# Kernel tuning notes

Hardware: AMD Instinct MI355X
Metric: run time of the kernel (lower is better)

Reference implementation:

```python
import jax, jax.numpy as jnp
import numpy as np

B, S, IN_SIZE = 16, 2000, 128
D, H, FF, OUT = 256, 2, 256, 64


def setup_inputs() -> dict:
    key = jax.random.key(0)
    ks = jax.random.split(key, 8)
    u = lambda k, shape: jax.random.uniform(k, shape, minval=-0.1, maxval=0.1, dtype=jnp.float32)
    g = lambda k, shape, fan: jax.random.normal(k, shape, dtype=jnp.float32) * (1.0 / np.sqrt(fan))
    return {
        "src": jax.random.normal(ks[0], (B, S, IN_SIZE), dtype=jnp.float32),
        "enc_w": u(ks[1], (D, IN_SIZE)), "enc_b": jnp.zeros((D,), jnp.float32),
        "in_proj_w": g(ks[2], (3 * D, D), D), "in_proj_b": jnp.zeros((3 * D,), jnp.float32),
        "out_proj_w": g(ks[3], (D, D), D), "out_proj_b": jnp.zeros((D,), jnp.float32),
        "ln1_g": jnp.ones((D,), jnp.float32), "ln1_b": jnp.zeros((D,), jnp.float32),
        "ff1_w": g(ks[4], (FF, D), D), "ff1_b": jnp.zeros((FF,), jnp.float32),
        "ff2_w": g(ks[5], (D, FF), FF), "ff2_b": jnp.zeros((D,), jnp.float32),
        "ln2_g": jnp.ones((D,), jnp.float32), "ln2_b": jnp.zeros((D,), jnp.float32),
        "dec_w": u(ks[6], (OUT, D)), "dec_b": jnp.zeros((OUT,), jnp.float32),
        "N": 100,
    }


def _pos_encoding(seq_len, d):
    pos = np.arange(seq_len, dtype=np.float32)[:, None]
    div = np.exp(np.arange(0, d, 2, dtype=np.float32) * (-np.log(10000.0) / d))
    pe = np.zeros((seq_len, d), np.float32)
    pe[:, 0::2] = np.sin(pos * div)
    pe[:, 1::2] = np.cos(pos * div)
    return jnp.asarray(pe)


def _layer_norm(x, g, b, eps=1e-5):
    m = x.mean(-1, keepdims=True)
    v = x.var(-1, keepdims=True)
    return (x - m) / jnp.sqrt(v + eps) * g + b


def reference(src, enc_w, enc_b, in_proj_w, in_proj_b, out_proj_w, out_proj_b,
              ln1_g, ln1_b, ff1_w, ff1_b, ff2_w, ff2_b, ln2_g, ln2_b,
              dec_w, dec_b, N):
    b, s, _ = src.shape
    d = enc_w.shape[0]
    h = H
    hd = d // h

    # linear encode + sinusoidal positional encoding (dropout inactive at eval)
    x = src @ enc_w.T + enc_b + _pos_encoding(s, d)[None]  # [B,S,D]

    # banded causal mask: row i attends to j in [i-N, i] (diagonal kept by initial triu)
    idx = jnp.arange(s)
    allowed = (idx[None, :] <= idx[:, None]) & (idx[None, :] >= idx[:, None] - N)
    mask = jnp.where(allowed, 0.0, -jnp.inf).astype(x.dtype)  # [S,S]

    # self-attention (torch MultiheadAttention: fused in_proj, scale 1/sqrt(head_dim))
    qkv = x @ in_proj_w.T + in_proj_b  # [B,S,3D]
    q, k, v = jnp.split(qkv, 3, axis=-1)
    heads = lambda t: t.reshape(b, s, h, hd)
    q = heads(q) * (1.0 / np.sqrt(hd))
    k, v = heads(k), heads(v)
    scores = jnp.einsum('bihd,bjhd->bhij', q, k) + mask  # [B,H,S,S]
    attn = jax.nn.softmax(scores, axis=-1)
    ctx = jnp.einsum('bhij,bjhd->bihd', attn, v).reshape(b, s, d)
    attn_out = ctx @ out_proj_w.T + out_proj_b

    # post-norm encoder layer (torch default): add&norm, relu FFN, add&norm
    x = _layer_norm(x + attn_out, ln1_g, ln1_b)
    ff = jax.nn.relu(x @ ff1_w.T + ff1_b) @ ff2_w.T + ff2_b
    x = _layer_norm(x + ff, ln2_g, ln2_b)

    return x @ dec_w.T + dec_b  # [B,S,OUT]
```

## Files before the change

kernel.cpp:

```cpp
#include <hip/hip_runtime.h>
#include <hip/hip_bf16.h>
#include <math.h>

#define BATCH 16
#define SEQ   2000
#define INSZ  128
#define DMODEL 256
#define NHEAD 2
#define HDIM  128
#define FFDIM 256
#define OUTSZ 64
#define MROWS (BATCH * SEQ)

#define TQ 32
#define TK 160
#define NQT ((SEQ + TQ - 1) / TQ)

typedef __attribute__((ext_vector_type(8))) short bf16x8;
typedef __attribute__((ext_vector_type(4))) float f32x4;

static __device__ __forceinline__ short f2bf(float f) {
    union { float f; unsigned int u; } c; c.f = f;
    unsigned int u = c.u + 0x7FFF + ((c.u >> 16) & 1);
    return (short)(u >> 16);
}
static __device__ __forceinline__ float bf2f(short s) {
    union { unsigned int u; float f; } c; c.u = ((unsigned int)(unsigned short)s) << 16;
    return c.f;
}

static __device__ __forceinline__ int xcd_swizzle(int bid, int nwg) {
    const int q = nwg >> 3, r = nwg & 7;
    const int xcd = bid & 7, pos = bid >> 3;
    return (xcd < r ? xcd * (q + 1) : r * (q + 1) + (xcd - r) * q) + pos;
}

__global__ __launch_bounds__(256) void setup_kernel(const float* __restrict__ w0,
                                                    const float* __restrict__ w1,
                                                    const float* __restrict__ w2,
                                                    const float* __restrict__ w3,
                                                    const float* __restrict__ w4,
                                                    const float* __restrict__ w5,
                                                    const float* __restrict__ inb,
                                                    float* __restrict__ pe,
                                                    short* __restrict__ wdst,
                                                    float* __restrict__ bdst) {
    const int blk = blockIdx.x;
    const int t = threadIdx.x;
    if (blk < SEQ) {
        const double c = -9.210340371976184 / 256.0;
        const double div = exp((double)(t & ~1) * c);
        const double ang = (double)blk * div;
        pe[(size_t)blk * DMODEL + t] = (float)((t & 1) ? cos(ang) : sin(ang));
    } else if (blk < SEQ + 1728) {
        const int idx = (blk - SEQ) * 256 + t;
        float v;
        if (idx < 32768) v = w0[idx];
        else if (idx < 229376) {
            const int e = idx - 32768;
            v = w1[e];
            if (e < 65536) v *= 0.08838834764831845f;
        }
        else if (idx < 294912) v = w2[idx - 229376];
        else if (idx < 360448) v = w3[idx - 294912];
        else if (idx < 425984) v = w4[idx - 360448];
        else                   v = w5[idx - 425984];
        wdst[idx] = f2bf(v);
    } else {
        const int i = (blk - SEQ - 1728) * 256 + t;
        bdst[i] = inb[i] * (i < 256 ? 0.08838834764831845f : 1.f);
    }
}

template <int EPI, bool ABF, bool OBF>
__global__ __launch_bounds__(256) void gemm_mfma_kernel(const void* __restrict__ Av,
                                                        const short* __restrict__ W,
                                                        const float* __restrict__ bias,
                                                        const float* __restrict__ pe,
                                                        void* __restrict__ Cv,
                                                        int M, int N, int K, int nbx) {
    __shared__ short As[128][72];
    __shared__ short Ws[64][72];

    const int bid = xcd_swizzle(blockIdx.x, gridDim.x);
    const int m0 = (bid / nbx) * 128;
    const int n0 = (bid % nbx) * 64;
    const int tid = threadIdx.x;
    const int wid = tid >> 6;
    const int wr = wid >> 1;
    const int wc = wid & 1;
    const int lane = tid & 63;
    const int lo = lane & 15;
    const int hi = lane >> 4;

    f32x4 acc[4][2];
    #pragma unroll
    for (int mt = 0; mt < 4; ++mt)
        #pragma unroll
        for (int nt = 0; nt < 2; ++nt) acc[mt][nt] = (f32x4){0.f, 0.f, 0.f, 0.f};

    for (int k0 = 0; k0 < K; k0 += 64) {
        if (ABF) {
            const short* A = (const short*)Av;
            #pragma unroll
            for (int l = 0; l < 4; ++l) {
                const int s = tid + 256 * l;
                const int r = s >> 3;
                const int c8 = s & 7;
                const bf16x8 v = *(const bf16x8*)(A + (size_t)(m0 + r) * K + k0 + c8 * 8);
                *(bf16x8*)&As[r][c8 * 8] = v;
            }
        } else {
            const float* A = (const float*)Av;
            #pragma unroll
            for (int l = 0; l < 8; ++l) {
                const int s = tid + 256 * l;
                const int r = s >> 4;
                const int c4 = s & 15;
                const float4 v = *(const float4*)(A + (size_t)(m0 + r) * K + k0 + c4 * 4);
                *(short4*)&As[r][c4 * 4] = make_short4(f2bf(v.x), f2bf(v.y), f2bf(v.z), f2bf(v.w));
            }
        }
        #pragma unroll
        for (int l = 0; l < 2; ++l) {
            const int s = tid + 256 * l;
            const int r = s >> 3;
            const int c8 = s & 7;
            const bf16x8 v = *(const bf16x8*)(W + (size_t)(n0 + r) * K + k0 + c8 * 8);
            *(bf16x8*)&Ws[r][c8 * 8] = v;
        }
        __syncthreads();

        #pragma unroll
        for (int kk = 0; kk < 2; ++kk) {
            bf16x8 bfr[2];
            #pragma unroll
            for (int nt = 0; nt < 2; ++nt)
                bfr[nt] = *(const bf16x8*)&Ws[wc * 32 + nt * 16 + lo][kk * 32 + hi * 8];
            #pragma unroll
            for (int mt = 0; mt < 4; ++mt) {
                const bf16x8 afr = *(const bf16x8*)&As[wr * 64 + mt * 16 + lo][kk * 32 + hi * 8];
                acc[mt][0] = __builtin_amdgcn_mfma_f32_16x16x32_bf16(afr, bfr[0], acc[mt][0], 0, 0, 0);
                acc[mt][1] = __builtin_amdgcn_mfma_f32_16x16x32_bf16(afr, bfr[1], acc[mt][1], 0, 0, 0);
            }
        }
        __syncthreads();
    }

    #pragma unroll
    for (int nt = 0; nt < 2; ++nt) {
        const int col = n0 + wc * 32 + nt * 16 + lo;
        const float bi = bias[col];
        #pragma unroll
        for (int mt = 0; mt < 4; ++mt) {
            #pragma unroll
            for (int r = 0; r < 4; ++r) {
                const int row = m0 + wr * 64 + mt * 16 + hi * 4 + r;
                float v = acc[mt][nt][r] + bi;
                if (EPI == 1) v = fmaxf(v, 0.f);
                if (EPI == 2) v += pe[(size_t)(row % SEQ) * DMODEL + col];
                if (OBF) ((short*)Cv)[(size_t)row * N + col] = f2bf(v);
                else     ((float*)Cv)[(size_t)row * N + col] = v;
            }
        }
    }
}

__global__ __launch_bounds__(256) void gemm_ln_kernel(const short* __restrict__ A,
                                                      const short* __restrict__ W,
                                                      const float* __restrict__ bias,
                                                      const short* __restrict__ R,
                                                      const float* __restrict__ g,
                                                      const float* __restrict__ beta,
                                                      short* __restrict__ out,
                                                      int M, int K) {
    __shared__ short As[64][72];
    __shared__ short Ws[256][72];
    __shared__ float rsum[64][2];
    __shared__ float rsq[64][2];

    const int tid = threadIdx.x;
    const int m0 = blockIdx.x * 64;
    const int wid = tid >> 6;
    const int wr = wid >> 1;
    const int wc = wid & 1;
    const int lane = tid & 63;
    const int lo = lane & 15;
    const int hi = lane >> 4;

    f32x4 acc[2][8];
    #pragma unroll
    for (int mt = 0; mt < 2; ++mt)
        #pragma unroll
        for (int nt = 0; nt < 8; ++nt) acc[mt][nt] = (f32x4){0.f, 0.f, 0.f, 0.f};

    for (int k0 = 0; k0 < K; k0 += 64) {
        #pragma unroll
        for (int l = 0; l < 2; ++l) {
            const int s = tid + 256 * l;
            const int r = s >> 3;
            const int c8 = s & 7;
            *(bf16x8*)&As[r][c8 * 8] = *(const bf16x8*)(A + (size_t)(m0 + r) * K + k0 + c8 * 8);
        }
        #pragma unroll
        for (int l = 0; l < 8; ++l) {
            const int s = tid + 256 * l;
            const int r = s >> 3;
            const int c8 = s & 7;
            *(bf16x8*)&Ws[r][c8 * 8] = *(const bf16x8*)(W + (size_t)r * K + k0 + c8 * 8);
        }
        __syncthreads();

        #pragma unroll
        for (int kk = 0; kk < 2; ++kk) {
            bf16x8 bfr[8];
            #pragma unroll
            for (int nt = 0; nt < 8; ++nt)
                bfr[nt] = *(const bf16x8*)&Ws[wc * 128 + nt * 16 + lo][kk * 32 + hi * 8];
            #pragma unroll
            for (int mt = 0; mt < 2; ++mt) {
                const bf16x8 afr = *(const bf16x8*)&As[wr * 32 + mt * 16 + lo][kk * 32 + hi * 8];
                #pragma unroll
                for (int nt = 0; nt < 8; ++nt)
                    acc[mt][nt] = __builtin_amdgcn_mfma_f32_16x16x32_bf16(afr, bfr[nt], acc[mt][nt], 0, 0, 0);
            }
        }
        __syncthreads();
    }

    float bi[8], gg[8], bb[8];
    #pragma unroll
    for (int nt = 0; nt < 8; ++nt) {
        const int col = wc * 128 + nt * 16 + lo;
        bi[nt] = bias[col]; gg[nt] = g[col]; bb[nt] = beta[col];
    }

    #pragma unroll
    for (int mt = 0; mt < 2; ++mt) {
        #pragma unroll
        for (int r = 0; r < 4; ++r) {
            const int rl = wr * 32 + mt * 16 + hi * 4 + r;
            const size_t grow = (size_t)(m0 + rl) * DMODEL;
            float s = 0.f, q = 0.f;
            #pragma unroll
            for (int nt = 0; nt < 8; ++nt) {
                const int col = wc * 128 + nt * 16 + lo;
                float v = acc[mt][nt][r] + bi[nt] + bf2f(R[grow + col]);
                acc[mt][nt][r] = v;
                s += v; q += v * v;
            }
            #pragma unroll
            for (int o = 1; o < 16; o <<= 1) { s += __shfl_xor(s, o); q += __shfl_xor(q, o); }
            if (lo == 0) { rsum[rl][wc] = s; rsq[rl][wc] = q; }
        }
    }
    __syncthreads();

    #pragma unroll
    for (int mt = 0; mt < 2; ++mt) {
        #pragma unroll
        for (int r = 0; r < 4; ++r) {
            const int rl = wr * 32 + mt * 16 + hi * 4 + r;
            const float mean = (rsum[rl][0] + rsum[rl][1]) * (1.f / DMODEL);
            const float var = (rsq[rl][0] + rsq[rl][1]) * (1.f / DMODEL) - mean * mean;
            const float rstd = rsqrtf(var + 1e-5f);
            const size_t grow = (size_t)(m0 + rl) * DMODEL;
            #pragma unroll
            for (int nt = 0; nt < 8; ++nt) {
                const int col = wc * 128 + nt * 16 + lo;
                out[grow + col] = f2bf((acc[mt][nt][r] - mean) * rstd * gg[nt] + bb[nt]);
            }
        }
    }
}

__global__ __launch_bounds__(256, 3) void attn_mfma_kernel(const short* __restrict__ qkv,
                                                           short* __restrict__ ctx,
                                                           const int* __restrict__ nptr) {
    __shared__ short KV[160 * 128];
    __shared__ short QP[32 * 160];
    __shared__ float redmax[2][32];
    __shared__ float redsum[2][32];

    const int tid = threadIdx.x;
    const int bid = xcd_swizzle(blockIdx.x, gridDim.x);
    const int tile = bid % NQT;
    const int bh = bid / NQT;
    const int h = bh & (NHEAD - 1);
    const int b = bh >> 1;
    const int NN = *nptr;
    const int i0 = tile * TQ;
    const int klo = max(0, i0 - NN);
    const size_t base = (size_t)b * SEQ * 768;

    const int lane = tid & 63;
    const int wid = tid >> 6;
    const int lo = lane & 15;
    const int hi = lane >> 4;
    const int wm = wid >> 1;
    const int wn = wid & 1;

    #pragma unroll
    for (int l = 0; l < 10; ++l) {
        const int s = tid + 256 * l;
        const int r = s >> 4;
        const int c8 = s & 15;
        const int j = min(klo + r, SEQ - 1);
        const bf16x8 v = *(const bf16x8*)(qkv + base + (size_t)j * 768 + DMODEL + h * HDIM + c8 * 8);
        *(bf16x8*)&KV[(r * 128 + c8 * 8) ^ ((r & 7) << 3)] = v;
    }
    #pragma unroll
    for (int l = 0; l < 2; ++l) {
        const int s = tid + 256 * l;
        const int r = s >> 4;
        const int c8 = s & 15;
        const int qi = min(i0 + r, SEQ - 1);
        const bf16x8 v = *(const bf16x8*)(qkv + base + (size_t)qi * 768 + h * HDIM + c8 * 8);
        *(bf16x8*)&QP[(r * 128 + c8 * 8) ^ ((r & 7) << 3)] = v;
    }
    __syncthreads();

    f32x4 sacc[5];
    #pragma unroll
    for (int mf = 0; mf < 5; ++mf) sacc[mf] = (f32x4){0.f, 0.f, 0.f, 0.f};
    #pragma unroll
    for (int ks = 0; ks < 4; ++ks) {
        const int qrow = wn * 16 + lo;
        const bf16x8 qf = *(const bf16x8*)&QP[(qrow * 128 + ks * 32 + hi * 8) ^ ((qrow & 7) << 3)];
        #pragma unroll
        for (int mf = 0; mf < 5; ++mf) {
            const int krow = wm * 80 + mf * 16 + lo;
            const bf16x8 kf = *(const bf16x8*)&KV[(krow * 128 + ks * 32 + hi * 8) ^ ((krow & 7) << 3)];
            sacc[mf] = __builtin_amdgcn_mfma_f32_16x16x32_bf16(kf, qf, sacc[mf], 0, 0, 0);
        }
    }

    const int qq = wn * 16 + lo;
    const int qi = i0 + qq;
    float mxw = -3.4e38f;
    #pragma unroll
    for (int mf = 0; mf < 5; ++mf)
        #pragma unroll
        for (int r = 0; r < 4; ++r) {
            const int ja = klo + wm * 80 + mf * 16 + hi * 4 + r;
            const bool ok = (ja >= qi - NN) && (ja <= qi);
            sacc[mf][r] = ok ? sacc[mf][r] : -3.4e38f;
            mxw = fmaxf(mxw, sacc[mf][r]);
        }
    mxw = fmaxf(mxw, __shfl_xor(mxw, 16));
    mxw = fmaxf(mxw, __shfl_xor(mxw, 32));
    mxw = fmaxf(mxw, -1e30f);
    float sml = 0.f;
    #pragma unroll
    for (int mf = 0; mf < 5; ++mf)
        #pragma unroll
        for (int r = 0; r < 4; ++r) {
            const float p = expf(sacc[mf][r] - mxw);
            sacc[mf][r] = p;
            sml += p;
        }
    sml += __shfl_xor(sml, 16);
    sml += __shfl_xor(sml, 32);
    if (hi == 0) { redmax[wm][qq] = mxw; redsum[wm][qq] = sml; }
    __syncthreads();

    #pragma unroll
    for (int l = 0; l < 10; ++l) {
        const int s = tid + 256 * l;
        const int r = s >> 4;
        const int c8 = s & 15;
        const int j = min(klo + r, SEQ - 1);
        const bf16x8 v = *(const bf16x8*)(qkv + base + (size_t)j * 768 + 2 * DMODEL + h * HDIM + c8 * 8);
        *(bf16x8*)&KV[(r * 128 + c8 * 8) ^ (((r >> 3) & 3) << 4)] = v;
    }

    {
        const float m0 = redmax[0][qq], m1 = redmax[1][qq];
        const float mx = fmaxf(m0, m1);
        const float tot = redsum[0][qq] * expf(m0 - mx) + redsum[1][qq] * expf(m1 - mx);
        const float fac = expf(mxw - mx) / tot;
        #pragma unroll
        for (int mf = 0; mf < 5; ++mf)
            #pragma unroll
            for (int r = 0; r < 4; ++r) {
                const int key = wm * 80 + mf * 16 + hi * 4 + r;
                QP[(qq * 160 + key) ^ ((qq & 3) << 3)] = f2bf(sacc[mf][r] * fac);
            }
    }
    __syncthreads();

    f32x4 oacc[2][2];
    #pragma unroll
    for (int mf = 0; mf < 2; ++mf)
        #pragma unroll
        for (int nf = 0; nf < 2; ++nf) oacc[mf][nf] = (f32x4){0.f, 0.f, 0.f, 0.f};
    const int dimb = wid * 32;
    #pragma unroll
    for (int ksp = 0; ksp < 5; ++ksp) {
        bf16x8 vf0, vf1;
        #pragma unroll
        for (int j = 0; j < 8; ++j) {
            const int key = ksp * 32 + hi * 8 + j;
            const int x = ((key >> 3) & 3) << 4;
            vf0[j] = KV[(key * 128 + dimb + lo) ^ x];
            vf1[j] = KV[(key * 128 + dimb + 16 + lo) ^ x];
        }
        #pragma unroll
        for (int mf = 0; mf < 2; ++mf) {
            const int prow = mf * 16 + lo;
            const bf16x8 pf = *(const bf16x8*)&QP[(prow * 160 + ksp * 32 + hi * 8) ^ ((prow & 3) << 3)];
            oacc[mf][0] = __builtin_amdgcn_mfma_f32_16x16x32_bf16(pf, vf0, oacc[mf][0], 0, 0, 0);
            oacc[mf][1] = __builtin_amdgcn_mfma_f32_16x16x32_bf16(pf, vf1, oacc[mf][1], 0, 0, 0);
        }
    }
    #pragma unroll
    for (int mf = 0; mf < 2; ++mf)
        #pragma unroll
        for (int r = 0; r < 4; ++r) {
            const int q = mf * 16 + hi * 4 + r;
            if (i0 + q < SEQ) {
                short* dst = ctx + ((size_t)b * SEQ + i0 + q) * DMODEL + h * HDIM + dimb;
                dst[lo]      = f2bf(oacc[mf][0][r]);
                dst[16 + lo] = f2bf(oacc[mf][1][r]);
            }
        }
}

extern "C" void kernel_launch(void* const* d_in, const int* in_sizes, int n_in,
                              void* d_out, int out_size, void* d_ws, size_t ws_size,
                              hipStream_t stream) {
    const float* src       = (const float*)d_in[0];
    const float* enc_w     = (const float*)d_in[1];
    const float* enc_b     = (const float*)d_in[2];
    const float* in_proj_w = (const float*)d_in[3];
    const float* in_proj_b = (const float*)d_in[4];
    const float* out_proj_w= (const float*)d_in[5];
    const float* out_proj_b= (const float*)d_in[6];
    const float* ln1_g     = (const float*)d_in[7];
    const float* ln1_b     = (const float*)d_in[8];
    const float* ff1_w     = (const float*)d_in[9];
    const float* ff1_b     = (const float*)d_in[10];
    const float* ff2_w     = (const float*)d_in[11];
    const float* ff2_b     = (const float*)d_in[12];
    const float* ln2_g     = (const float*)d_in[13];
    const float* ln2_b     = (const float*)d_in[14];
    const float* dec_w     = (const float*)d_in[15];
    const float* dec_b     = (const float*)d_in[16];
    const int*   nptr      = (const int*)d_in[17];

    short* SW   = (short*)d_ws;
    short* X    = SW;
    short* QKV  = SW + 8192000;
    short* CTX  = SW + 32768000;
    float* PE   = (float*)(SW + 49152000);
    short* WB   = SW + 50176000;
    float* QKVB = (float*)(SW + 50618368);
    short* X1   = CTX;
    short* FFH  = QKV;
    short* X2   = X;
    float* OUT  = (float*)d_out;

    short* enc_wb  = WB;
    short* inp_wb  = WB + 32768;
    short* outp_wb = WB + 229376;
    short* ff1_wb  = WB + 294912;
    short* ff2_wb  = WB + 360448;
    short* dec_wb  = WB + 425984;

    setup_kernel<<<SEQ + 1728 + 3, 256, 0, stream>>>(
        enc_w, in_proj_w, out_proj_w, ff1_w, ff2_w, dec_w, in_proj_b,
        PE, WB, QKVB);

    gemm_mfma_kernel<2, false, true><<<(MROWS / 128) * (DMODEL / 64), 256, 0, stream>>>(
        src, enc_wb, enc_b, PE, X, MROWS, DMODEL, INSZ, DMODEL / 64);
    gemm_mfma_kernel<0, true, true><<<(MROWS / 128) * ((3 * DMODEL) / 64), 256, 0, stream>>>(
        X, inp_wb, QKVB, nullptr, QKV, MROWS, 3 * DMODEL, DMODEL, (3 * DMODEL) / 64);
    attn_mfma_kernel<<<BATCH * NHEAD * NQT, 256, 0, stream>>>(QKV, CTX, nptr);
    gemm_ln_kernel<<<MROWS / 64, 256, 0, stream>>>(
        CTX, outp_wb, out_proj_b, X, ln1_g, ln1_b, X1, MROWS, DMODEL);
    gemm_mfma_kernel<1, true, true><<<(MROWS / 128) * (FFDIM / 64), 256, 0, stream>>>(
        X1, ff1_wb, ff1_b, nullptr, FFH, MROWS, FFDIM, DMODEL, FFDIM / 64);
    gemm_ln_kernel<<<MROWS / 64, 256, 0, stream>>>(
        FFH, ff2_wb, ff2_b, X1, ln2_g, ln2_b, X2, MROWS, FFDIM);
    gemm_mfma_kernel<0, true, false><<<(MROWS / 128) * (OUTSZ / 64), 256, 0, stream>>>(
        X2, dec_wb, dec_b, nullptr, OUT, MROWS, OUTSZ, DMODEL, OUTSZ / 64);
}
```

Before: 210.2 us.

## Fuse out-proj, LayerNorm, FFN, LayerNorm and decoder into one per-row-tile kernel

Replaces the four post-attention launches (out-proj+LN1, FF1 with ReLU, FF2+LN2, decoder) with a single kernel. Each block handles 32 rows and keeps the intermediate activations in shared memory, so the X1, FFH and X2 tensors never go through global memory. The cost is that every block reloads all weight matrices through LDS for only 32 rows, and the 32-row tile leaves fewer MFMA tiles per wave, so weight traffic and sync overhead per row go up.

Measured after the change: 202.5 us. 3.6% less time.

```diff
diff --git a/kernel.cpp b/kernel.cpp
--- a/kernel.cpp
+++ b/kernel.cpp
@@ -72,12 +72,12 @@
     }
 }
 
-template <int EPI, bool ABF, bool OBF>
+template <int EPI, bool ABF>
 __global__ __launch_bounds__(256) void gemm_mfma_kernel(const void* __restrict__ Av,
                                                         const short* __restrict__ W,
                                                         const float* __restrict__ bias,
                                                         const float* __restrict__ pe,
-                                                        void* __restrict__ Cv,
+                                                        short* __restrict__ C,
                                                         int M, int N, int K, int nbx) {
     __shared__ short As[128][72];
     __shared__ short Ws[64][72];
@@ -107,8 +107,7 @@
                 const int s = tid + 256 * l;
                 const int r = s >> 3;
                 const int c8 = s & 7;
-                const bf16x8 v = *(const bf16x8*)(A + (size_t)(m0 + r) * K + k0 + c8 * 8);
-                *(bf16x8*)&As[r][c8 * 8] = v;
+                *(bf16x8*)&As[r][c8 * 8] = *(const bf16x8*)(A + (size_t)(m0 + r) * K + k0 + c8 * 8);
             }
         } else {
             const float* A = (const float*)Av;
@@ -126,8 +125,7 @@
             const int s = tid + 256 * l;
             const int r = s >> 3;
             const int c8 = s & 7;
-            const bf16x8 v = *(const bf16x8*)(W + (size_t)(n0 + r) * K + k0 + c8 * 8);
-            *(bf16x8*)&Ws[r][c8 * 8] = v;
+            *(bf16x8*)&Ws[r][c8 * 8] = *(const bf16x8*)(W + (size_t)(n0 + r) * K + k0 + c8 * 8);
         }
         __syncthreads();
 
@@ -157,30 +155,36 @@
             for (int r = 0; r < 4; ++r) {
                 const int row = m0 + wr * 64 + mt * 16 + hi * 4 + r;
                 float v = acc[mt][nt][r] + bi;
-                if (EPI == 1) v = fmaxf(v, 0.f);
                 if (EPI == 2) v += pe[(size_t)(row % SEQ) * DMODEL + col];
-                if (OBF) ((short*)Cv)[(size_t)row * N + col] = f2bf(v);
-                else     ((float*)Cv)[(size_t)row * N + col] = v;
-            }
-        }
-    }
-}
-
-__global__ __launch_bounds__(256) void gemm_ln_kernel(const short* __restrict__ A,
-                                                      const short* __restrict__ W,
-                                                      const float* __restrict__ bias,
-                                                      const short* __restrict__ R,
-                                                      const float* __restrict__ g,
-                                                      const float* __restrict__ beta,
-                                                      short* __restrict__ out,
-                                                      int M, int K) {
-    __shared__ short As[64][72];
+                C[(size_t)row * N + col] = f2bf(v);
+            }
+        }
+    }
+}
+
+__global__ __launch_bounds__(256) void tail_fused_kernel(const short* __restrict__ CTX,
+                                                         const short* __restrict__ X,
+                                                         const short* __restrict__ Wo,
+                                                         const float* __restrict__ bo,
+                                                         const float* __restrict__ g1,
+                                                         const float* __restrict__ be1,
+                                                         const short* __restrict__ W1,
+                                                         const float* __restrict__ bF1,
+                                                         const short* __restrict__ W2,
+                                                         const float* __restrict__ bF2,
+                                                         const float* __restrict__ g2,
+                                                         const float* __restrict__ be2,
+                                                         const short* __restrict__ Wd,
+                                                         const float* __restrict__ bd,
+                                                         float* __restrict__ out) {
     __shared__ short Ws[256][72];
-    __shared__ float rsum[64][2];
-    __shared__ float rsq[64][2];
+    __shared__ short Abuf[4][32][72];
+    __shared__ short Xbuf[4][32][72];
+    __shared__ float rsum[32][2];
+    __shared__ float rsq[32][2];
 
     const int tid = threadIdx.x;
-    const int m0 = blockIdx.x * 64;
+    const int m0 = blockIdx.x * 32;
     const int wid = tid >> 6;
     const int wr = wid >> 1;
     const int wc = wid & 1;
@@ -188,90 +192,172 @@
     const int lo = lane & 15;
     const int hi = lane >> 4;
 
-    f32x4 acc[2][8];
-    #pragma unroll
-    for (int mt = 0; mt < 2; ++mt)
-        #pragma unroll
-        for (int nt = 0; nt < 8; ++nt) acc[mt][nt] = (f32x4){0.f, 0.f, 0.f, 0.f};
-
-    for (int k0 = 0; k0 < K; k0 += 64) {
-        #pragma unroll
-        for (int l = 0; l < 2; ++l) {
-            const int s = tid + 256 * l;
-            const int r = s >> 3;
-            const int c8 = s & 7;
-            *(bf16x8*)&As[r][c8 * 8] = *(const bf16x8*)(A + (size_t)(m0 + r) * K + k0 + c8 * 8);
-        }
-        #pragma unroll
-        for (int l = 0; l < 8; ++l) {
-            const int s = tid + 256 * l;
-            const int r = s >> 3;
-            const int c8 = s & 7;
-            *(bf16x8*)&Ws[r][c8 * 8] = *(const bf16x8*)(W + (size_t)r * K + k0 + c8 * 8);
-        }
-        __syncthreads();
-
-        #pragma unroll
-        for (int kk = 0; kk < 2; ++kk) {
-            bf16x8 bfr[8];
-            #pragma unroll
-            for (int nt = 0; nt < 8; ++nt)
-                bfr[nt] = *(const bf16x8*)&Ws[wc * 128 + nt * 16 + lo][kk * 32 + hi * 8];
-            #pragma unroll
-            for (int mt = 0; mt < 2; ++mt) {
-                const bf16x8 afr = *(const bf16x8*)&As[wr * 32 + mt * 16 + lo][kk * 32 + hi * 8];
-                #pragma unroll
-                for (int nt = 0; nt < 8; ++nt)
-                    acc[mt][nt] = __builtin_amdgcn_mfma_f32_16x16x32_bf16(afr, bfr[nt], acc[mt][nt], 0, 0, 0);
-            }
-        }
-        __syncthreads();
-    }
-
-    float bi[8], gg[8], bb[8];
-    #pragma unroll
-    for (int nt = 0; nt < 8; ++nt) {
-        const int col = wc * 128 + nt * 16 + lo;
-        bi[nt] = bias[col]; gg[nt] = g[col]; bb[nt] = beta[col];
-    }
-
-    #pragma unroll
-    for (int mt = 0; mt < 2; ++mt) {
-        #pragma unroll
-        for (int r = 0; r < 4; ++r) {
-            const int rl = wr * 32 + mt * 16 + hi * 4 + r;
+    #pragma unroll
+    for (int l = 0; l < 4; ++l) {
+        const int s = tid + 256 * l;
+        const int r = s >> 5;
+        const int c8 = s & 31;
+        *(bf16x8*)&Abuf[c8 >> 3][r][(c8 & 7) * 8] =
+            *(const bf16x8*)(CTX + (size_t)(m0 + r) * DMODEL + c8 * 8);
+    }
+    __syncthreads();
+
+    f32x4 acc[8];
+
+    #define STAGE_K256(BUF, WG)                                                          \
+    {                                                                                    \
+        _Pragma("unroll") for (int nt = 0; nt < 8; ++nt) acc[nt] = (f32x4){0,0,0,0};     \
+        for (int kt = 0; kt < 4; ++kt) {                                                 \
+            _Pragma("unroll") for (int l = 0; l < 8; ++l) {                              \
+                const int s = tid + 256 * l;                                             \
+                const int rr = s >> 3, c8 = s & 7;                                       \
+                *(bf16x8*)&Ws[rr][c8 * 8] =                                              \
+                    *(const bf16x8*)((WG) + (size_t)rr * 256 + kt * 64 + c8 * 8);        \
+            }                                                                            \
+            __syncthreads();                                                             \
+            _Pragma("unroll") for (int kk = 0; kk < 2; ++kk) {                           \
+                bf16x8 bfr[8];                                                           \
+                _Pragma("unroll") for (int nt = 0; nt < 8; ++nt)                         \
+                    bfr[nt] = *(const bf16x8*)&Ws[wc * 128 + nt * 16 + lo][kk * 32 + hi * 8]; \
+                const bf16x8 afr = *(const bf16x8*)&BUF[kt][wr * 16 + lo][kk * 32 + hi * 8]; \
+                _Pragma("unroll") for (int nt = 0; nt < 8; ++nt)                         \
+                    acc[nt] = __builtin_amdgcn_mfma_f32_16x16x32_bf16(afr, bfr[nt], acc[nt], 0, 0, 0); \
+            }                                                                            \
+            __syncthreads();                                                             \
+        }                                                                                \
+    }
+
+    STAGE_K256(Abuf, Wo)
+    {
+        float bi[8], gg[8], bb[8];
+        #pragma unroll
+        for (int nt = 0; nt < 8; ++nt) {
+            const int col = wc * 128 + nt * 16 + lo;
+            bi[nt] = bo[col]; gg[nt] = g1[col]; bb[nt] = be1[col];
+        }
+        #pragma unroll
+        for (int r = 0; r < 4; ++r) {
+            const int rl = wr * 16 + hi * 4 + r;
             const size_t grow = (size_t)(m0 + rl) * DMODEL;
             float s = 0.f, q = 0.f;
             #pragma unroll
             for (int nt = 0; nt < 8; ++nt) {
                 const int col = wc * 128 + nt * 16 + lo;
-                float v = acc[mt][nt][r] + bi[nt] + bf2f(R[grow + col]);
-                acc[mt][nt][r] = v;
+                float v = acc[nt][r] + bi[nt] + bf2f(X[grow + col]);
+                acc[nt][r] = v;
                 s += v; q += v * v;
             }
             #pragma unroll
             for (int o = 1; o < 16; o <<= 1) { s += __shfl_xor(s, o); q += __shfl_xor(q, o); }
             if (lo == 0) { rsum[rl][wc] = s; rsq[rl][wc] = q; }
         }
-    }
-    __syncthreads();
-
-    #pragma unroll
-    for (int mt = 0; mt < 2; ++mt) {
-        #pragma unroll
-        for (int r = 0; r < 4; ++r) {
-            const int rl = wr * 32 + mt * 16 + hi * 4 + r;
+        __syncthreads();
+        #pragma unroll
+        for (int r = 0; r < 4; ++r) {
+            const int rl = wr * 16 + hi * 4 + r;
             const float mean = (rsum[rl][0] + rsum[rl][1]) * (1.f / DMODEL);
             const float var = (rsq[rl][0] + rsq[rl][1]) * (1.f / DMODEL) - mean * mean;
             const float rstd = rsqrtf(var + 1e-5f);
-            const size_t grow = (size_t)(m0 + rl) * DMODEL;
             #pragma unroll
             for (int nt = 0; nt < 8; ++nt) {
                 const int col = wc * 128 + nt * 16 + lo;
-                out[grow + col] = f2bf((acc[mt][nt][r] - mean) * rstd * gg[nt] + bb[nt]);
-            }
-        }
-    }
+                Xbuf[col >> 6][rl][col & 63] = f2bf((acc[nt][r] - mean) * rstd * gg[nt] + bb[nt]);
+            }
+        }
+    }
+    __syncthreads();
+
+    STAGE_K256(Xbuf, W1)
+    {
+        #pragma unroll
+        for (int nt = 0; nt < 8; ++nt) {
+            const int col = wc * 128 + nt * 16 + lo;
+            const float bi = bF1[col];
+            #pragma unroll
+            for (int r = 0; r < 4; ++r) {
+                const int rl = wr * 16 + hi * 4 + r;
+                Abuf[col >> 6][rl][col & 63] = f2bf(fmaxf(acc[nt][r] + bi, 0.f));
+            }
+        }
+    }
+    __syncthreads();
+
+    STAGE_K256(Abuf, W2)
+    {
+        float bi[8], gg[8], bb[8];
+        #pragma unroll
+        for (int nt = 0; nt < 8; ++nt) {
+            const int col = wc * 128 + nt * 16 + lo;
+            bi[nt] = bF2[col]; gg[nt] = g2[col]; bb[nt] = be2[col];
+        }
+        #pragma unroll
+        for (int r = 0; r < 4; ++r) {
+            const int rl = wr * 16 + hi * 4 + r;
+            float s = 0.f, q = 0.f;
+            #pragma unroll
+            for (int nt = 0; nt < 8; ++nt) {
+                const int col = wc * 128 + nt * 16 + lo;
+                float v = acc[nt][r] + bi[nt] + bf2f(Xbuf[col >> 6][rl][col & 63]);
+                acc[nt][r] = v;
+                s += v; q += v * v;
+            }
+            #pragma unroll
+            for (int o = 1; o < 16; o <<= 1) { s += __shfl_xor(s, o); q += __shfl_xor(q, o); }
+            if (lo == 0) { rsum[rl][wc] = s; rsq[rl][wc] = q; }
+        }
+        __syncthreads();
+        #pragma unroll
+        for (int r = 0; r < 4; ++r) {
+            const int rl = wr * 16 + hi * 4 + r;
+            const float mean = (rsum[rl][0] + rsum[rl][1]) * (1.f / DMODEL);
+            const float var = (rsq[rl][0] + rsq[rl][1]) * (1.f / DMODEL) - mean * mean;
+            const float rstd = rsqrtf(var + 1e-5f);
+            #pragma unroll
+            for (int nt = 0; nt < 8; ++nt) {
+                const int col = wc * 128 + nt * 16 + lo;
+                Xbuf[col >> 6][rl][col & 63] = f2bf((acc[nt][r] - mean) * rstd * gg[nt] + bb[nt]);
+            }
+        }
+    }
+    __syncthreads();
+
+    {
+        f32x4 acc2[2];
+        #pragma unroll
+        for (int nt = 0; nt < 2; ++nt) acc2[nt] = (f32x4){0.f, 0.f, 0.f, 0.f};
+        for (int kt = 0; kt < 4; ++kt) {
+            #pragma unroll
+            for (int l = 0; l < 2; ++l) {
+                const int s = tid + 256 * l;
+                const int rr = s >> 3, c8 = s & 7;
+                *(bf16x8*)&Ws[rr][c8 * 8] = *(const bf16x8*)(Wd + (size_t)rr * 256 + kt * 64 + c8 * 8);
+            }
+            __syncthreads();
+            #pragma unroll
+            for (int kk = 0; kk < 2; ++kk) {
+                bf16x8 bfr[2];
+                #pragma unroll
+                for (int nt = 0; nt < 2; ++nt)
+                    bfr[nt] = *(const bf16x8*)&Ws[wc * 32 + nt * 16 + lo][kk * 32 + hi * 8];
+                const bf16x8 afr = *(const bf16x8*)&Xbuf[kt][wr * 16 + lo][kk * 32 + hi * 8];
+                #pragma unroll
+                for (int nt = 0; nt < 2; ++nt)
+                    acc2[nt] = __builtin_amdgcn_mfma_f32_16x16x32_bf16(afr, bfr[nt], acc2[nt], 0, 0, 0);
+            }
+            __syncthreads();
+        }
+        #pragma unroll
+        for (int nt = 0; nt < 2; ++nt) {
+            const int col = wc * 32 + nt * 16 + lo;
+            const float bi = bd[col];
+            #pragma unroll
+            for (int r = 0; r < 4; ++r) {
+                const int row = m0 + wr * 16 + hi * 4 + r;
+                out[(size_t)row * OUTSZ + col] = acc2[nt][r] + bi;
+            }
+        }
+    }
+    #undef STAGE_K256
 }
 
 __global__ __launch_bounds__(256, 3) void attn_mfma_kernel(const short* __restrict__ qkv,
@@ -455,9 +541,6 @@
     float* PE   = (float*)(SW + 49152000);
     short* WB   = SW + 50176000;
     float* QKVB = (float*)(SW + 50618368);
-    short* X1   = CTX;
-    short* FFH  = QKV;
-    short* X2   = X;
     float* OUT  = (float*)d_out;
 
     short* enc_wb  = WB;
@@ -471,17 +554,13 @@
         enc_w, in_proj_w, out_proj_w, ff1_w, ff2_w, dec_w, in_proj_b,
         PE, WB, QKVB);
 
-    gemm_mfma_kernel<2, false, true><<<(MROWS / 128) * (DMODEL / 64), 256, 0, stream>>>(
+    gemm_mfma_kernel<2, false><<<(MROWS / 128) * (DMODEL / 64), 256, 0, stream>>>(
         src, enc_wb, enc_b, PE, X, MROWS, DMODEL, INSZ, DMODEL / 64);
-    gemm_mfma_kernel<0, true, true><<<(MROWS / 128) * ((3 * DMODEL) / 64), 256, 0, stream>>>(
+    gemm_mfma_kernel<0, true><<<(MROWS / 128) * ((3 * DMODEL) / 64), 256, 0, stream>>>(
         X, inp_wb, QKVB, nullptr, QKV, MROWS, 3 * DMODEL, DMODEL, (3 * DMODEL) / 64);
     attn_mfma_kernel<<<BATCH * NHEAD * NQT, 256, 0, stream>>>(QKV, CTX, nptr);
-    gemm_ln_kernel<<<MROWS / 64, 256, 0, stream>>>(
-        CTX, outp_wb, out_proj_b, X, ln1_g, ln1_b, X1, MROWS, DMODEL);
-    gemm_mfma_kernel<1, true, true><<<(MROWS / 128) * (FFDIM / 64), 256, 0, stream>>>(
-        X1, ff1_wb, ff1_b, nullptr, FFH, MROWS, FFDIM, DMODEL, FFDIM / 64);
-    gemm_ln_kernel<<<MROWS / 64, 256, 0, stream>>>(
-        FFH, ff2_wb, ff2_b, X1, ln2_g, ln2_b, X2, MROWS, FFDIM);
-    gemm_mfma_kernel<0, true, false><<<(MROWS / 128) * (OUTSZ / 64), 256, 0, stream>>>(
-        X2, dec_wb, dec_b, nullptr, OUT, MROWS, OUTSZ, DMODEL, OUTSZ / 64);
-}
+    tail_fused_kernel<<<MROWS / 32, 256, 0, stream>>>(
+        CTX, X, outp_wb, out_proj_b, ln1_g, ln1_b,
+        ff1_wb, ff1_b, ff2_wb, ff2_b, ln2_g, ln2_b,
+        dec_wb, dec_b, OUT);
+}
```
